# Optimization experiments

Hardware: AMD Instinct MI355X
Metric: run time of the kernel (lower is better)

## Reference

```python
import jax, jax.numpy as jnp
import numpy as np

N_SENSORY = 784   # MNIST sensory nodes (init_modes prints 784)
LR_X = 0.5        # lr_x
T = 10            # T_test fixed-point iterations


def setup_inputs() -> dict:
    key = jax.random.key(0)
    k1, k2, k3, k4 = jax.random.split(key, 4)
    B, N, E = 128, 2000, 131072
    x = jax.random.normal(k1, (B, N), dtype=jnp.float32)
    src = jax.random.randint(k2, (E,), 0, N)
    tgt = jax.random.randint(k3, (E,), 0, N)
    edge_index = jnp.stack([src, tgt]).astype(jnp.int32)  # [2, E], shared across batch
    # w init: fill 0.001 + 1e-4 noise (see _reset_params), gathered per-edge
    w_edges = (0.001 + 0.0001 * jax.random.normal(k4, (E,), dtype=jnp.float32))
    # test mode: update internal + supervised nodes (>= 784); sensory errors zeroed
    # because use_input_error=False -> same mask used for errors.
    update_mask = (jnp.arange(N) >= N_SENSORY).astype(jnp.float32)
    return {"x": x, "edge_index": edge_index, "w_edges": w_edges,
            "update_mask": update_mask}


def reference(x, edge_index, w_edges, update_mask):
    # x: [B, N] node values; edge_index: [2, E] (row 0 = source, row 1 = target)
    src, tgt = edge_index[0], edge_index[1]
    N = x.shape[1]

    seg = lambda vals, idx: jax.ops.segment_sum(vals, idx, num_segments=N)
    dfdx = lambda v: 1.0 - jnp.tanh(v) ** 2  # tanh_derivative

    def step(xc, _):
        fx = jnp.tanh(xc)
        # PredictionMessagePassing (flow=target_to_source, aggr=add):
        #   mu[src] += f(x[tgt]) * w_edge
        mu = jax.vmap(lambda fb: seg(fb[tgt] * w_edges, src))(fx)       # [B, N]
        # use_input_error=False: sensory errors zeroed
        err = (xc - mu) * update_mask                                    # [B, N]
        # GradientMessagePassing (flow=source_to_target, aggr=add):
        #   aggr[tgt] += dfdx(x[tgt]) * err[src] * w_edge ; dx = err - aggr
        agg = jax.vmap(lambda eb: seg(eb[src] * w_edges, tgt))(err)      # [B, N]
        dx = err - dfdx(xc) * agg
        # gradient step on unclamped (internal + label) nodes only
        xc = xc - LR_X * dx * update_mask
        return xc, None

    x_final, _ = jax.lax.scan(step, x, None, length=T)
    return x_final
```

## Files before the change

### kernel.cpp

```cpp
#include <hip/hip_runtime.h>

#define NITER 10
#define NBLK 250
#define HB 32
#define CAP_H 96


__device__ __forceinline__ uint32_t aload(const uint32_t* p) {
  return __hip_atomic_load(p, __ATOMIC_RELAXED, __HIP_MEMORY_SCOPE_AGENT);
}
__device__ __forceinline__ void astore(uint32_t* p, uint32_t v) {
  __hip_atomic_store(p, v, __ATOMIC_RELAXED, __HIP_MEMORY_SCOPE_AGENT);
}
__device__ __forceinline__ float bf2f_lo(uint32_t v) { return __uint_as_float(v << 16); }
__device__ __forceinline__ float bf2f_hi(uint32_t v) { return __uint_as_float(v & 0xFFFF0000u); }
__device__ __forceinline__ uint32_t f2bf_bits(float f) {
  uint32_t b = __float_as_uint(f);
  b += 0x7FFFu + ((b >> 16) & 1u);
  return b >> 16;
}
__device__ __forceinline__ uint32_t pack_bf16x2(float lo, float hi) {
  return f2bf_bits(lo) | (f2bf_bits(hi) << 16);
}

__device__ __forceinline__ void gbar(uint32_t* slots, uint32_t* gen, uint32_t target) {
  asm volatile("s_waitcnt vmcnt(0)" ::: "memory");
  __syncthreads();
  if (blockIdx.x == 0) {
    if (threadIdx.x < 64) {
      for (;;) {
        bool ok = true;
        for (int i = threadIdx.x; i < NBLK; i += 64)
          ok &= (i == 0) || (aload(&slots[i]) >= target);
        if (__all(ok)) break;
        __builtin_amdgcn_s_sleep(1);
      }
      if (threadIdx.x == 0) astore(gen, target);
    }
  } else {
    if (threadIdx.x == 0) {
      astore(&slots[blockIdx.x], target);
      while (aload(gen) < target) __builtin_amdgcn_s_sleep(2);
    }
  }
  __syncthreads();
  asm volatile("" ::: "memory");
}

__device__ __forceinline__ void gq_lds(const uint32_t* __restrict__ se, int len,
                                       const uint32_t* buf, int lane, float& o0, float& o1) {
  float a0[8], a1[8];
#pragma unroll
  for (int j = 0; j < 8; ++j) { a0[j] = 0.f; a1[j] = 0.f; }
#pragma unroll 2
  for (int p = 0; p < len; p += 8) {
    uint32_t e[8];
#pragma unroll
    for (int j = 0; j < 8; ++j) e[j] = se[p + j];
    uint32_t v[8];
#pragma unroll
    for (int j = 0; j < 8; ++j) v[j] = aload(&buf[((e[j] & 0xFFFFu) << 6) + lane]);
#pragma unroll
    for (int j = 0; j < 8; ++j) {
      float wj = __uint_as_float(e[j] & 0xFFFF0000u);
      a0[j] = fmaf(wj, bf2f_lo(v[j]), a0[j]);
      a1[j] = fmaf(wj, bf2f_hi(v[j]), a1[j]);
    }
  }
  o0 = ((a0[0] + a0[1]) + (a0[2] + a0[3])) + ((a0[4] + a0[5]) + (a0[6] + a0[7]));
  o1 = ((a1[0] + a1[1]) + (a1[2] + a1[3])) + ((a1[4] + a1[5]) + (a1[6] + a1[7]));
}

__device__ __forceinline__ void gq_glb(const uint32_t* __restrict__ ed, int len,
                                       const uint32_t* buf, int lane, float& o0, float& o1) {
  float a0[8], a1[8];
#pragma unroll
  for (int j = 0; j < 8; ++j) { a0[j] = 0.f; a1[j] = 0.f; }
#pragma unroll 2
  for (int p = 0; p < len; p += 8) {
    uint32_t e[8], v[8];
#pragma unroll
    for (int j = 0; j < 8; ++j) {
      bool ok = (p + j) < len;
      e[j] = ok ? aload(&ed[p + j]) : 0u;
      v[j] = ok ? aload(&buf[((e[j] & 0xFFFFu) << 6) + lane]) : 0u;
    }
#pragma unroll
    for (int j = 0; j < 8; ++j) {
      float wj = __uint_as_float(e[j] & 0xFFFF0000u);
      a0[j] = fmaf(wj, bf2f_lo(v[j]), a0[j]);
      a1[j] = fmaf(wj, bf2f_hi(v[j]), a1[j]);
    }
  }
  o0 = ((a0[0] + a0[1]) + (a0[2] + a0[3])) + ((a0[4] + a0[5]) + (a0[6] + a0[7]));
  o1 = ((a1[0] + a1[1]) + (a1[2] + a1[3])) + ((a1[4] + a1[5]) + (a1[6] + a1[7]));
}


__global__ __launch_bounds__(1024, 4) void pc_all(
    const float* __restrict__ x, float* __restrict__ out,
    const int* __restrict__ src, const int* __restrict__ tgt,
    const float* __restrict__ w, const float* __restrict__ mask,
    int* __restrict__ partS, int* __restrict__ partT,
    int* __restrict__ offS, int* __restrict__ offT,
    int* __restrict__ curS, int* __restrict__ curT,
    int* __restrict__ actv, int* __restrict__ nactg,
    uint32_t* __restrict__ edgeS, uint32_t* __restrict__ edgeT,
    uint32_t* fx32, uint32_t* err32, uint32_t* barbuf, int E, int N) {
  __shared__ int h[4096];
  __shared__ uint32_t sE[2][16][CAP_H];
  __shared__ float2 psum[8][64];
  uint32_t* slots = barbuf;
  uint32_t* gen = barbuf + 288;

  const int bid = blockIdx.x, tid = threadIdx.x;
  const int wid = tid >> 6, lane = tid & 63;

  if (bid < HB) {
    for (int i = tid; i < 2 * N; i += 1024) h[i] = 0;
    __syncthreads();
    const int chunk = (E + HB - 1) / HB;
    const int base = bid * chunk;
    const int end = min(base + chunk, E);
    for (int e = base + tid; e < end; e += 1024) {
      int s = src[e], t = tgt[e];
      if (mask[s] != 0.f) {
        atomicAdd(&h[s], 1);
        if (mask[t] != 0.f) atomicAdd(&h[N + t], 1);
      }
    }
    __syncthreads();
    for (int i = tid; i < N; i += 1024) {
      astore((uint32_t*)&partS[bid * 2048 + i], (uint32_t)h[i]);
      astore((uint32_t*)&partT[bid * 2048 + i], (uint32_t)h[N + i]);
    }
  }
  gbar(slots, gen, 1);

  if (bid < 3) {
    int* tsum = h;
    int v2[2];
    int s = 0;
#pragma unroll
    for (int i2 = 0; i2 < 2; ++i2) {
      int idx = tid * 2 + i2;
      int c = 0;
      if (idx < N) {
        if (bid == 2) {
          c = (mask[idx] != 0.f) ? 1 : 0;
        } else {
          const uint32_t* part = (const uint32_t*)(bid ? partT : partS);
          for (int k = 0; k < HB; ++k) c += (int)aload(&part[k * 2048 + idx]);
        }
      }
      v2[i2] = s;
      s += c;
    }
    __syncthreads();
    tsum[tid] = s;
    __syncthreads();
    for (int d = 1; d < 1024; d <<= 1) {
      int t = (tid >= d) ? tsum[tid - d] : 0;
      __syncthreads();
      tsum[tid] += t;
      __syncthreads();
    }
    int tbase = tsum[tid] - s;
    if (bid == 2) {
#pragma unroll
      for (int i2 = 0; i2 < 2; ++i2) {
        int idx = tid * 2 + i2;
        if (idx < N && mask[idx] != 0.f)
          astore((uint32_t*)&actv[tbase + v2[i2]], (uint32_t)idx);
      }
      if (tid == 1023) astore((uint32_t*)nactg, (uint32_t)tsum[1023]);
    } else {
      int* off = bid ? offT : offS;
      int* cur = bid ? curT : curS;
#pragma unroll
      for (int i2 = 0; i2 < 2; ++i2) {
        int idx = tid * 2 + i2;
        if (idx < N) {
          int o = tbase + v2[i2];
          astore((uint32_t*)&off[idx], (uint32_t)o);
          astore((uint32_t*)&cur[idx], (uint32_t)o);
        } else if (idx == N) {
          astore((uint32_t*)&off[idx], (uint32_t)(tbase + v2[i2]));
        }
      }
    }
  }
  gbar(slots, gen, 2);

  {
    const int chunk = (E + NBLK - 1) / NBLK;
    const int base = bid * chunk;
    const int end = min(base + chunk, E);
    for (int e = base + tid; e < end; e += 1024) {
      int s = src[e], t = tgt[e];
      if (mask[s] != 0.f) {
        uint32_t wb = __float_as_uint(w[e]);
        wb = (wb + 0x7FFFu + ((wb >> 16) & 1u)) & 0xFFFF0000u;
        int p = atomicAdd(&curS[s], 1);
        astore(&edgeS[p], (uint32_t)t | wb);
        if (mask[t] != 0.f) {
          int q = atomicAdd(&curT[t], 1);
          astore(&edgeT[q], (uint32_t)s | wb);
        }
      }
    }
  }

  const int ps = wid >> 1, sub = wid & 1;
  const int nact = (int)aload((const uint32_t*)nactg);
  const int p = ps * NBLK + bid;
  const bool act = (p < nact);
  int n = 0, i = 0, aS = 0, qlS = 0, qpS = 0, aT = 0, qlT = 0, qpT = 0;
  bool fS = true, fT = true;
  float m = 0.f, x0 = 0.f, x1 = 0.f, fx0 = 0.f, fx1 = 0.f, e0 = 0.f, e1 = 0.f;

  if (act) {
    n = (int)aload((const uint32_t*)&actv[p]);
    i = (n << 6) + lane;
    const uint32_t* offSu = (const uint32_t*)offS;
    const uint32_t* offTu = (const uint32_t*)offT;
    const int s0 = (int)aload(&offSu[n]), degS = (int)aload(&offSu[n + 1]) - s0;
    const int t0 = (int)aload(&offTu[n]), degT = (int)aload(&offTu[n + 1]) - t0;
    aS = s0 + ((degS * sub) >> 1); qlS = (s0 + ((degS * (sub + 1)) >> 1)) - aS;
    aT = t0 + ((degT * sub) >> 1); qlT = (t0 + ((degT * (sub + 1)) >> 1)) - aT;
    qpS = (qlS + 7) & ~7; qpT = (qlT + 7) & ~7;
    fS = (qpS <= CAP_H); fT = (qpT <= CAP_H);
    if (sub == 0) {
      m = mask[n];
      x0 = x[(2 * lane) * N + n];
      x1 = x[(2 * lane + 1) * N + n];
      fx0 = tanhf(x0);
      fx1 = tanhf(x1);
      astore(&fx32[i], pack_bf16x2(fx0, fx1));
    }
  }
  for (int g = bid * 1024 + tid; g < N * 64; g += NBLK * 1024) {
    int nn = g >> 6;
    if (mask[nn] == 0.f) {
      int l = g & 63;
      astore(&fx32[g], pack_bf16x2(tanhf(x[(2 * l) * N + nn]), tanhf(x[(2 * l + 1) * N + nn])));
    }
  }
  for (int g = bid * 1024 + tid; g < N * 128; g += NBLK * 1024) {
    int b = g / N, nn = g - b * N;
    if (mask[nn] == 0.f) out[g] = x[g];
  }
  gbar(slots, gen, 3);

  if (act) {
    if (fS)
      for (int k = lane; k < qpS; k += 64) sE[0][wid][k] = (k < qlS) ? aload(&edgeS[aS + k]) : 0u;
    if (fT)
      for (int k = lane; k < qpT; k += 64) sE[1][wid][k] = (k < qlT) ? aload(&edgeT[aT + k]) : 0u;
  }

  uint32_t g = 3;
  for (int it = 0; it < NITER; ++it) {
    float p0 = 0.f, p1 = 0.f;
    if (act) {
      if (fS) gq_lds(&sE[0][wid][0], qpS, fx32, lane, p0, p1);
      else    gq_glb(edgeS + aS, qlS, fx32, lane, p0, p1);
      if (sub) psum[ps][lane] = make_float2(p0, p1);
    }
    __syncthreads();
    if (act && sub == 0) {
      float2 q = psum[ps][lane];
      e0 = (x0 - (p0 + q.x)) * m;
      e1 = (x1 - (p1 + q.y)) * m;
      astore(&err32[i], pack_bf16x2(e0, e1));
    }
    gbar(slots, gen, ++g);

    if (act) {
      if (fT) gq_lds(&sE[1][wid][0], qpT, err32, lane, p0, p1);
      else    gq_glb(edgeT + aT, qlT, err32, lane, p0, p1);
      if (sub) psum[ps][lane] = make_float2(p0, p1);
    }
    __syncthreads();
    if (act && sub == 0) {
      float2 q = psum[ps][lane];
      const float ag0 = p0 + q.x, ag1 = p1 + q.y;
      const float dx0 = e0 - (1.f - fx0 * fx0) * ag0;
      const float dx1 = e1 - (1.f - fx1 * fx1) * ag1;
      x0 -= 0.5f * dx0 * m;
      x1 -= 0.5f * dx1 * m;
      fx0 = tanhf(x0);
      fx1 = tanhf(x1);
      if (it < NITER - 1) astore(&fx32[i], pack_bf16x2(fx0, fx1));
    }
    if (it < NITER - 1) gbar(slots, gen, ++g);
  }

  if (act && sub == 0) {
    out[(2 * lane) * N + n] = x0;
    out[(2 * lane + 1) * N + n] = x1;
  }
}


extern "C" void kernel_launch(void* const* d_in, const int* in_sizes, int n_in,
                              void* d_out, int out_size, void* d_ws, size_t ws_size,
                              hipStream_t stream) {
  const float* x = (const float*)d_in[0];
  const int* ei = (const int*)d_in[1];
  const float* w = (const float*)d_in[2];
  const float* mask = (const float*)d_in[3];
  int E = in_sizes[2];
  int N = in_sizes[3];
  const int* src = ei;
  const int* tgt = ei + E;
  float* out = (float*)d_out;

  size_t off = 0;
  auto alloc = [&](size_t bytes) -> void* {
    off = (off + 255) & ~(size_t)255;
    void* p = (char*)d_ws + off;
    off += bytes;
    return p;
  };
  uint32_t* edgeS = (uint32_t*)alloc((size_t)E * 4);
  uint32_t* edgeT = (uint32_t*)alloc((size_t)E * 4);
  int* partS = (int*)alloc((size_t)HB * 2048 * 4);
  int* partT = (int*)alloc((size_t)HB * 2048 * 4);
  int* offS = (int*)alloc(2048 * 4);
  int* offT = (int*)alloc(2048 * 4);
  int* curS = (int*)alloc(2048 * 4);
  int* curT = (int*)alloc(2048 * 4);
  int* actv = (int*)alloc(2048 * 4);
  int* nactg = (int*)alloc(64 * 4);
  uint32_t* fx32 = (uint32_t*)alloc((size_t)N * 64 * 4);
  uint32_t* err32 = (uint32_t*)alloc((size_t)N * 64 * 4);
  uint32_t* barbuf = (uint32_t*)alloc(512 * 4);

  hipMemsetAsync(barbuf, 0, 512 * 4, stream);

  pc_all<<<NBLK, 1024, 0, stream>>>(x, out, src, tgt, w, mask, partS, partT, offS, offT,
                                    curS, curT, actv, nactg, edgeS, edgeT, fx32, err32,
                                    barbuf, E, N);
}
```

Before: 163.5 us.

## Use per-iteration fx/err buffers so gathers can use plain cached loads

Measured after the change: 160.8 us. About the same (-1.7%).

```diff
diff --git a/kernel.cpp b/kernel.cpp
--- a/kernel.cpp
+++ b/kernel.cpp
@@ -47,6 +47,14 @@
   asm volatile("" ::: "memory");
 }
 
+
+template <bool L2M>
+__device__ __forceinline__ uint32_t mload(const uint32_t* p) {
+  if constexpr (L2M) return *p;
+  else return aload(p);
+}
+
+template <bool L2M>
 __device__ __forceinline__ void gq_lds(const uint32_t* __restrict__ se, int len,
                                        const uint32_t* buf, int lane, float& o0, float& o1) {
   float a0[8], a1[8];
@@ -59,7 +67,7 @@
     for (int j = 0; j < 8; ++j) e[j] = se[p + j];
     uint32_t v[8];
 #pragma unroll
-    for (int j = 0; j < 8; ++j) v[j] = aload(&buf[((e[j] & 0xFFFFu) << 6) + lane]);
+    for (int j = 0; j < 8; ++j) v[j] = mload<L2M>(&buf[((e[j] & 0xFFFFu) << 6) + lane]);
 #pragma unroll
     for (int j = 0; j < 8; ++j) {
       float wj = __uint_as_float(e[j] & 0xFFFF0000u);
@@ -71,6 +79,7 @@
   o1 = ((a1[0] + a1[1]) + (a1[2] + a1[3])) + ((a1[4] + a1[5]) + (a1[6] + a1[7]));
 }
 
+template <bool L2M>
 __device__ __forceinline__ void gq_glb(const uint32_t* __restrict__ ed, int len,
                                        const uint32_t* buf, int lane, float& o0, float& o1) {
   float a0[8], a1[8];
@@ -83,7 +92,7 @@
     for (int j = 0; j < 8; ++j) {
       bool ok = (p + j) < len;
       e[j] = ok ? aload(&ed[p + j]) : 0u;
-      v[j] = ok ? aload(&buf[((e[j] & 0xFFFFu) << 6) + lane]) : 0u;
+      v[j] = ok ? mload<L2M>(&buf[((e[j] & 0xFFFFu) << 6) + lane]) : 0u;
     }
 #pragma unroll
     for (int j = 0; j < 8; ++j) {
@@ -97,6 +106,7 @@
 }
 
 
+template <bool L2M>
 __global__ __launch_bounds__(1024, 4) void pc_all(
     const float* __restrict__ x, float* __restrict__ out,
     const int* __restrict__ src, const int* __restrict__ tgt,
@@ -115,6 +125,9 @@
 
   const int bid = blockIdx.x, tid = threadIdx.x;
   const int wid = tid >> 6, lane = tid & 63;
+  const int row = N * 64;
+  const int fstr = L2M ? row : 0;
+  const int estr = L2M ? row : 0;
 
   if (bid < HB) {
     for (int i = tid; i < 2 * N; i += 1024) h[i] = 0;
@@ -239,11 +252,16 @@
       astore(&fx32[i], pack_bf16x2(fx0, fx1));
     }
   }
-  for (int g = bid * 1024 + tid; g < N * 64; g += NBLK * 1024) {
+  for (int g = bid * 1024 + tid; g < row; g += NBLK * 1024) {
     int nn = g >> 6;
     if (mask[nn] == 0.f) {
       int l = g & 63;
-      astore(&fx32[g], pack_bf16x2(tanhf(x[(2 * l) * N + nn]), tanhf(x[(2 * l + 1) * N + nn])));
+      uint32_t pv = pack_bf16x2(tanhf(x[(2 * l) * N + nn]), tanhf(x[(2 * l + 1) * N + nn]));
+      if constexpr (L2M) {
+        for (int k = 0; k < NITER; ++k) astore(&fx32[(size_t)k * row + g], pv);
+      } else {
+        astore(&fx32[g], pv);
+      }
     }
   }
   for (int g = bid * 1024 + tid; g < N * 128; g += NBLK * 1024) {
@@ -261,10 +279,12 @@
 
   uint32_t g = 3;
   for (int it = 0; it < NITER; ++it) {
+    const uint32_t* Fk = fx32 + (size_t)it * fstr;
+    uint32_t* Ek = err32 + (size_t)it * estr;
     float p0 = 0.f, p1 = 0.f;
     if (act) {
-      if (fS) gq_lds(&sE[0][wid][0], qpS, fx32, lane, p0, p1);
-      else    gq_glb(edgeS + aS, qlS, fx32, lane, p0, p1);
+      if (fS) gq_lds<L2M>(&sE[0][wid][0], qpS, Fk, lane, p0, p1);
+      else    gq_glb<L2M>(edgeS + aS, qlS, Fk, lane, p0, p1);
       if (sub) psum[ps][lane] = make_float2(p0, p1);
     }
     __syncthreads();
@@ -272,13 +292,13 @@
       float2 q = psum[ps][lane];
       e0 = (x0 - (p0 + q.x)) * m;
       e1 = (x1 - (p1 + q.y)) * m;
-      astore(&err32[i], pack_bf16x2(e0, e1));
+      astore(&Ek[i], pack_bf16x2(e0, e1));
     }
     gbar(slots, gen, ++g);
 
     if (act) {
-      if (fT) gq_lds(&sE[1][wid][0], qpT, err32, lane, p0, p1);
-      else    gq_glb(edgeT + aT, qlT, err32, lane, p0, p1);
+      if (fT) gq_lds<L2M>(&sE[1][wid][0], qpT, Ek, lane, p0, p1);
+      else    gq_glb<L2M>(edgeT + aT, qlT, Ek, lane, p0, p1);
       if (sub) psum[ps][lane] = make_float2(p0, p1);
     }
     __syncthreads();
@@ -291,7 +311,7 @@
       x1 -= 0.5f * dx1 * m;
       fx0 = tanhf(x0);
       fx1 = tanhf(x1);
-      if (it < NITER - 1) astore(&fx32[i], pack_bf16x2(fx0, fx1));
+      if (it < NITER - 1) astore(&fx32[(size_t)(it + 1) * fstr + i], pack_bf16x2(fx0, fx1));
     }
     if (it < NITER - 1) gbar(slots, gen, ++g);
   }
@@ -333,13 +353,28 @@
   int* curT = (int*)alloc(2048 * 4);
   int* actv = (int*)alloc(2048 * 4);
   int* nactg = (int*)alloc(64 * 4);
-  uint32_t* fx32 = (uint32_t*)alloc((size_t)N * 64 * 4);
-  uint32_t* err32 = (uint32_t*)alloc((size_t)N * 64 * 4);
   uint32_t* barbuf = (uint32_t*)alloc(512 * 4);
 
+  const size_t row = (size_t)N * 64 * 4;
+  bool l2mode = (off + 2 * (size_t)NITER * row + 512) <= ws_size;
+  uint32_t* fx32, *err32;
+  if (l2mode) {
+    fx32 = (uint32_t*)alloc((size_t)NITER * row);
+    err32 = (uint32_t*)alloc((size_t)NITER * row);
+  } else {
+    fx32 = (uint32_t*)alloc(row);
+    err32 = (uint32_t*)alloc(row);
+  }
+
   hipMemsetAsync(barbuf, 0, 512 * 4, stream);
 
-  pc_all<<<NBLK, 1024, 0, stream>>>(x, out, src, tgt, w, mask, partS, partT, offS, offT,
-                                    curS, curT, actv, nactg, edgeS, edgeT, fx32, err32,
-                                    barbuf, E, N);
-}
+  if (l2mode) {
+    pc_all<true><<<NBLK, 1024, 0, stream>>>(x, out, src, tgt, w, mask, partS, partT, offS, offT,
+                                            curS, curT, actv, nactg, edgeS, edgeT, fx32, err32,
+                                            barbuf, E, N);
+  } else {
+    pc_all<false><<<NBLK, 1024, 0, stream>>>(x, out, src, tgt, w, mask, partS, partT, offS, offT,
+                                             curS, curT, actv, nactg, edgeS, edgeT, fx32, err32,
+                                             barbuf, E, N);
+  }
+}
```
